# Performance work log

Hardware: AMD Instinct MI355X
Metric: run time of the kernel (lower is better)

Reference implementation:

```python
import jax, jax.numpy as jnp
import numpy as np

B, L, H = 2, 1024, 1024   # batch, seq_len, hidden_size
NH, D, K = 16, 64, 4      # num_heads, head_dim, conv kernel
HD = NH * D


def setup_inputs() -> dict:
    key = jax.random.key(0)
    ks = jax.random.split(key, 12)
    s = 0.02  # LeCun-ish init scale as in the torch module
    return {
        "hidden_states": jax.random.normal(ks[0], (B, L, H), jnp.float32),
        "Wq": jax.random.normal(ks[1], (HD, H), jnp.float32) * s,
        "bq": jnp.zeros((HD,), jnp.float32),
        "Wk": jax.random.normal(ks[2], (HD, H), jnp.float32) * s,
        "bk": jnp.zeros((HD,), jnp.float32),
        "Wv": jax.random.normal(ks[3], (HD, H), jnp.float32) * s,
        "bv": jnp.zeros((HD,), jnp.float32),
        "Wa": jax.random.normal(ks[4], (NH, H), jnp.float32) * s,
        "Wb": jax.random.normal(ks[5], (NH, H), jnp.float32) * s,
        "Wconv": jax.random.normal(ks[6], (HD, 1, K), jnp.float32) * s,
        "Wo": jax.random.normal(ks[7], (H, HD), jnp.float32) * s,
        "bo": jnp.zeros((H,), jnp.float32),
    }


def _gated_delta(q, k, v, alpha, beta):
    # q,k,v: [B,L,NH,D]; alpha,beta: [B,L,NH]
    # S_t = S_{t-1} @ (alpha_t * (I - beta_t k_t k_t^T)) + beta_t v_t k_t^T ; o_t = S_t q_t
    eye = jnp.eye(q.shape[-1], dtype=q.dtype)

    def step(S, xs):
        q_t, k_t, v_t, a_t, b_t = xs  # [B,NH,D], [B,NH]
        kk = jnp.einsum('bhd,bhe->bhde', k_t, k_t)
        decay = a_t[..., None, None] * (eye - b_t[..., None, None] * kk)
        S = jnp.einsum('bhde,bhef->bhdf', S, decay) \
            + b_t[..., None, None] * jnp.einsum('bhd,bhe->bhde', v_t, k_t)
        o_t = jnp.einsum('bhde,bhe->bhd', S, q_t)
        return S, o_t

    xs = (jnp.moveaxis(q, 1, 0), jnp.moveaxis(k, 1, 0), jnp.moveaxis(v, 1, 0),
          jnp.moveaxis(alpha, 1, 0), jnp.moveaxis(beta, 1, 0))
    S0 = jnp.zeros((q.shape[0], q.shape[2], q.shape[3], q.shape[3]), q.dtype)
    _, outs = jax.lax.scan(step, S0, xs)  # [L,B,NH,D]
    return jnp.transpose(outs, (1, 2, 0, 3))  # [B,NH,L,D] (matches torch stack+transposes)


def reference(hidden_states, Wq, bq, Wk, bk, Wv, bv, Wa, Wb, Wconv, Wo, bo):
    Bc, Lc, Hc = hidden_states.shape
    q = (hidden_states @ Wq.T + bq).reshape(Bc, Lc, NH, D)
    k = (hidden_states @ Wk.T + bk).reshape(Bc, Lc, NH, D)
    v = (hidden_states @ Wv.T + bv).reshape(Bc, Lc, NH, D)
    alpha = jax.nn.sigmoid(hidden_states @ Wa.T)   # [B,L,NH]
    beta = jax.nn.softplus(hidden_states @ Wb.T)   # [B,L,NH]

    out = _gated_delta(q, k, v, alpha, beta)       # [B,NH,L,D]
    out = out.reshape(Bc, Lc, NH * D)              # replicates torch's reshape of [B,NH,L,D]
    x = jnp.transpose(out, (0, 2, 1))              # [B,HD,L]
    conv = jax.lax.conv_general_dilated(
        x, Wconv, window_strides=(1,), padding=[(K - 1, 0)],
        feature_group_count=NH * D, dimension_numbers=('NCH', 'OIH', 'NCH'))
    x = x + conv                                   # residual depthwise causal conv
    x = jnp.transpose(x, (0, 2, 1))                # [B,L,HD]
    return x @ Wo.T + bo                           # [B,L,H]; dropout is identity at eval
```

## Files before the change

### kernel.cpp

```cpp
#include <hip/hip_runtime.h>
#include <math.h>

#define BB 2
#define LL 1024
#define HH 1024
#define NH 16
#define DD 64
#define HD (NH * DD)
#define MM (BB * LL)
#define RCT 32
#define KEXT 3072
#define NB_QKV 3200

typedef _Float16 f16x8 __attribute__((ext_vector_type(8)));
typedef _Float16 f16x4 __attribute__((ext_vector_type(4)));
typedef float f32x4 __attribute__((ext_vector_type(4)));

__device__ __forceinline__ void load_lds16(const void* g, void* l) {
    __builtin_amdgcn_global_load_lds(
        (const __attribute__((address_space(1))) void*)g,
        (__attribute__((address_space(3))) void*)l, 16, 0, 0);
}

__global__ __launch_bounds__(256) void convert_front(
    const float* __restrict__ hs,
    const float* __restrict__ Wq, const float* __restrict__ Wk,
    const float* __restrict__ Wv, const float* __restrict__ Wa,
    const float* __restrict__ Wb, const float* __restrict__ Wo,
    _Float16* __restrict__ Ae, _Float16* __restrict__ Be,
    _Float16* __restrict__ Be2)
{
    const int blk = blockIdx.x;
    const int t = threadIdx.x;

    if (blk >= 5248) {
        const int n = blk - 5248;
        float4 x = *(const float4*)(Wo + (size_t)n * 1024 + t * 4);
        f16x4 h;
        h[0] = (_Float16)(x.x * 64.f);
        h[1] = (_Float16)(x.y * 64.f);
        h[2] = (_Float16)(x.z * 64.f);
        h[3] = (_Float16)(x.w * 64.f);
        *(f16x4*)(Be2 + (size_t)n * 1024 + t * 4) = h;
        return;
    }

    const float* src = nullptr;
    _Float16* dst;
    float scale;
    bool a_side;
    if (blk < 2048) {
        src = hs + (size_t)blk * 1024;
        dst = Ae + (size_t)blk * KEXT;
        scale = 16.f; a_side = true;
    } else {
        const int n = blk - 2048;
        if (n < 1024)      src = Wq + (size_t)n * 1024;
        else if (n < 2048) src = Wk + (size_t)(n - 1024) * 1024;
        else if (n < 3072) src = Wv + (size_t)(n - 2048) * 1024;
        else if (n < 3088) src = Wa + (size_t)(n - 3072) * 1024;
        else if (n < 3104) src = Wb + (size_t)(n - 3088) * 1024;
        dst = Be + (size_t)n * KEXT;
        scale = 64.f; a_side = false;
    }
    float4 x = src ? *(const float4*)(src + t * 4) : make_float4(0.f,0.f,0.f,0.f);
    x.x *= scale; x.y *= scale; x.z *= scale; x.w *= scale;
    f16x4 h, l;
    h[0] = (_Float16)x.x; l[0] = (_Float16)(x.x - (float)h[0]);
    h[1] = (_Float16)x.y; l[1] = (_Float16)(x.y - (float)h[1]);
    h[2] = (_Float16)x.z; l[2] = (_Float16)(x.z - (float)h[2]);
    h[3] = (_Float16)x.w; l[3] = (_Float16)(x.w - (float)h[3]);
    _Float16* base = dst + t * 4;
    *(f16x4*)(base)        = h;
    *(f16x4*)(base + 1024) = a_side ? l : h;
    *(f16x4*)(base + 2048) = a_side ? h : l;
}

__global__ __launch_bounds__(256) void mfma_gemm_qkv(
    const _Float16* __restrict__ Ae, const _Float16* __restrict__ Be,
    float* __restrict__ qkv, float* __restrict__ ab,
    const float* __restrict__ bq, const float* __restrict__ bk,
    const float* __restrict__ bv)
{
    __shared__ __align__(16) _Float16 As[2][128 * 32];
    __shared__ __align__(16) _Float16 Bs[2][128 * 32];

    const int tid = threadIdx.x;
    const int wave = tid >> 6;
    const int lane = tid & 63;
    const int bm = blockIdx.y * 128;
    const int bn = blockIdx.x * 128;
    const int wr = (wave >> 1) * 64;
    const int wc = (wave & 1) * 64;

    const int srow = lane >> 2;
    const int scol = (lane & 3) * 8;
    const _Float16* gA0 = Ae + (size_t)(bm + wave * 32 + srow) * KEXT + scol;
    const _Float16* gA1 = gA0 + (size_t)16 * KEXT;
    const _Float16* gB0 = Be + (size_t)(bn + wave * 32 + srow) * KEXT + scol;
    const _Float16* gB1 = gB0 + (size_t)16 * KEXT;
    _Float16* lA0_0 = &As[0][(wave * 32) * 32];
    _Float16* lA1_0 = &As[0][(wave * 32 + 16) * 32];
    _Float16* lB0_0 = &Bs[0][(wave * 32) * 32];
    _Float16* lB1_0 = &Bs[0][(wave * 32 + 16) * 32];
    _Float16* lA0_1 = &As[1][(wave * 32) * 32];
    _Float16* lA1_1 = &As[1][(wave * 32 + 16) * 32];
    _Float16* lB0_1 = &Bs[1][(wave * 32) * 32];
    _Float16* lB1_1 = &Bs[1][(wave * 32 + 16) * 32];

    const int fm = lane & 15;
    const int fq = (lane >> 4) * 8;

    f32x4 acc[4][4] = {};

    for (int k0 = 0; k0 < KEXT; k0 += 64) {
        load_lds16(gA0 + k0,      lA0_0);
        load_lds16(gA1 + k0,      lA1_0);
        load_lds16(gB0 + k0,      lB0_0);
        load_lds16(gB1 + k0,      lB1_0);
        load_lds16(gA0 + k0 + 32, lA0_1);
        load_lds16(gA1 + k0 + 32, lA1_1);
        load_lds16(gB0 + k0 + 32, lB0_1);
        load_lds16(gB1 + k0 + 32, lB1_1);
        __syncthreads();

        #pragma unroll
        for (int s = 0; s < 2; ++s) {
            f16x8 a[4], b[4];
            #pragma unroll
            for (int mt = 0; mt < 4; ++mt)
                a[mt] = *(const f16x8*)&As[s][(wr + mt * 16 + fm) * 32 + fq];
            #pragma unroll
            for (int nt = 0; nt < 4; ++nt)
                b[nt] = *(const f16x8*)&Bs[s][(wc + nt * 16 + fm) * 32 + fq];
            #pragma unroll
            for (int mt = 0; mt < 4; ++mt)
                #pragma unroll
                for (int nt = 0; nt < 4; ++nt)
                    acc[mt][nt] = __builtin_amdgcn_mfma_f32_16x16x32_f16(
                        a[mt], b[nt], acc[mt][nt], 0, 0, 0);
        }
        __syncthreads();
    }

    const int rquad = (lane >> 4) * 4;
    #pragma unroll
    for (int mt = 0; mt < 4; ++mt) {
        #pragma unroll
        for (int nt = 0; nt < 4; ++nt) {
            const int col = bn + wc + nt * 16 + fm;
            #pragma unroll
            for (int i = 0; i < 4; ++i) {
                const int row = bm + wr + mt * 16 + rquad + i;
                float val = acc[mt][nt][i] * (1.0f / 1024.0f);
                if (col < 1024)
                    qkv[(size_t)row * 3072 + col] = val + bq[col];
                else if (col < 2048)
                    qkv[(size_t)row * 3072 + col] = val + bk[col - 1024];
                else if (col < 3072)
                    qkv[(size_t)row * 3072 + col] = val + bv[col - 2048];
                else {
                    const int c = col - 3072;
                    if (c < 16)
                        ab[(size_t)row * 32 + c] = 1.f / (1.f + expf(-val));
                    else if (c < 32)
                        ab[(size_t)row * 32 + c] =
                            fmaxf(val, 0.f) + log1pf(expf(-fabsf(val)));
                }
            }
        }
    }
}

__global__ __launch_bounds__(256) void mfma_gemm_out(
    const _Float16* __restrict__ Ae2, const _Float16* __restrict__ Be2,
    float* __restrict__ outp, const float* __restrict__ bo)
{
    __shared__ __align__(16) _Float16 As[2][128 * 32];
    __shared__ __align__(16) _Float16 Bs[2][64 * 32];

    const int tid = threadIdx.x;
    const int wave = tid >> 6;
    const int lane = tid & 63;
    const int bm = blockIdx.y * 128;
    const int bn = blockIdx.x * 64;
    const int wr = (wave >> 1) * 64;
    const int wc = (wave & 1) * 32;

    const int srow = lane >> 2;
    const int scol = (lane & 3) * 8;
    const _Float16* gA0 = Ae2 + (size_t)(bm + wave * 32 + srow) * 1024 + scol;
    const _Float16* gA1 = gA0 + (size_t)16 * 1024;
    const _Float16* gB0 = Be2 + (size_t)(bn + wave * 16 + srow) * 1024 + scol;
    _Float16* lA0_0 = &As[0][(wave * 32) * 32];
    _Float16* lA1_0 = &As[0][(wave * 32 + 16) * 32];
    _Float16* lB0_0 = &Bs[0][(wave * 16) * 32];
    _Float16* lA0_1 = &As[1][(wave * 32) * 32];
    _Float16* lA1_1 = &As[1][(wave * 32 + 16) * 32];
    _Float16* lB0_1 = &Bs[1][(wave * 16) * 32];

    const int fm = lane & 15;
    const int fq = (lane >> 4) * 8;

    f32x4 acc[4][2] = {};

    for (int k0 = 0; k0 < 1024; k0 += 64) {
        load_lds16(gA0 + k0,      lA0_0);
        load_lds16(gA1 + k0,      lA1_0);
        load_lds16(gB0 + k0,      lB0_0);
        load_lds16(gA0 + k0 + 32, lA0_1);
        load_lds16(gA1 + k0 + 32, lA1_1);
        load_lds16(gB0 + k0 + 32, lB0_1);
        __syncthreads();

        #pragma unroll
        for (int s = 0; s < 2; ++s) {
            f16x8 a[4], b[2];
            #pragma unroll
            for (int mt = 0; mt < 4; ++mt)
                a[mt] = *(const f16x8*)&As[s][(wr + mt * 16 + fm) * 32 + fq];
            #pragma unroll
            for (int nt = 0; nt < 2; ++nt)
                b[nt] = *(const f16x8*)&Bs[s][(wc + nt * 16 + fm) * 32 + fq];
            #pragma unroll
            for (int mt = 0; mt < 4; ++mt)
                #pragma unroll
                for (int nt = 0; nt < 2; ++nt)
                    acc[mt][nt] = __builtin_amdgcn_mfma_f32_16x16x32_f16(
                        a[mt], b[nt], acc[mt][nt], 0, 0, 0);
        }
        __syncthreads();
    }

    const int rquad = (lane >> 4) * 4;
    #pragma unroll
    for (int mt = 0; mt < 4; ++mt) {
        #pragma unroll
        for (int nt = 0; nt < 2; ++nt) {
            const int col = bn + wc + nt * 16 + fm;
            #pragma unroll
            for (int i = 0; i < 4; ++i) {
                const int row = bm + wr + mt * 16 + rquad + i;
                outp[(size_t)row * 1024 + col] = acc[mt][nt][i] * 64.f + bo[col];
            }
        }
    }
}

template <int CTRL>
__device__ __forceinline__ float dpp_addf(float x) {
    int y = __builtin_amdgcn_update_dpp(0, __builtin_bit_cast(int, x),
                                        CTRL, 0xF, 0xF, true);
    return x + __builtin_bit_cast(float, y);
}
__device__ __forceinline__ float red16(float x) {
    x = dpp_addf<0xB1>(x);
    x = dpp_addf<0x4E>(x);
    x = dpp_addf<0x124>(x);
    x = dpp_addf<0x128>(x);
    return x;
}

__global__ __launch_bounds__(64) void gdn_recurrence(
    const float* __restrict__ qkv, const float* __restrict__ ab,
    float* __restrict__ att)
{
    __shared__ __align__(16) float ks[2][RCT][64];
    __shared__ __align__(16) float qs[2][RCT][64];
    __shared__ __align__(16) float vs_[2][RCT][4];
    __shared__ __align__(16) float gab[2][RCT][2];

    const int blk = blockIdx.x;
    const int bh = blk & 31;
    const int s  = blk >> 5;
    const int b  = bh >> 4;
    const int h  = bh & 15;
    const int lane = threadIdx.x;
    const int rl = lane >> 4;
    const int el = lane & 15;
    const int e0 = el * 4;
    const int r0 = s * 4;

    const float* qb  = qkv + (size_t)b * LL * 3072 + h * 64;
    const float* kb  = qb + 1024;
    const float* vb  = qb + 2048 + r0;
    const float* abp = ab + (size_t)b * LL * 32 + h;
    float* op = att + ((size_t)(b * NH + h) * DD + r0 + rl) * LL;

    const int st = lane >> 4;
    const int sd = (lane & 15) * 4;

    float S0 = 0.f, S1 = 0.f, S2 = 0.f, S3 = 0.f;

    {
        const size_t ro = (size_t)st * 3072 + sd;
        #pragma unroll
        for (int m = 0; m < 8; ++m) {
            load_lds16(kb + ro + (size_t)m * 4 * 3072, &ks[0][m * 4][0]);
            load_lds16(qb + ro + (size_t)m * 4 * 3072, &qs[0][m * 4][0]);
        }
        float4 pv = make_float4(0.f,0.f,0.f,0.f);
        if (lane < RCT) pv = *(const float4*)(vb + (size_t)lane * 3072);
        float pab = (lane < 32) ? abp[(size_t)lane * 32]
                                : abp[(size_t)(lane - 32) * 32 + 16];
        if (lane < RCT) *(float4*)&vs_[0][lane][0] = pv;
        if (lane < 32) gab[0][lane][0] = pab;
        else           gab[0][lane - 32][1] = pab;
    }
    __syncthreads();

    const int NCHUNK = LL / RCT;
    for (int c = 0; c < NCHUNK; ++c) {
        const int cur = c & 1, nxt = cur ^ 1;
        const bool more = (c + 1 < NCHUNK);

        float4 pv = make_float4(0.f,0.f,0.f,0.f);
        float pab = 0.f;
        if (more) {
            const size_t t0 = (size_t)(c + 1) * RCT;
            const size_t ro = (t0 + st) * 3072 + sd;
            #pragma unroll
            for (int m = 0; m < 8; ++m) {
                load_lds16(kb + ro + (size_t)m * 4 * 3072, &ks[nxt][m * 4][0]);
                load_lds16(qb + ro + (size_t)m * 4 * 3072, &qs[nxt][m * 4][0]);
            }
            if (lane < RCT) pv = *(const float4*)(vb + (t0 + lane) * 3072);
            pab = (lane < 32) ? abp[(t0 + lane) * 32]
                              : abp[(t0 + lane - 32) * 32 + 16];
        }

        float4 kc = *(const float4*)&ks[cur][0][e0];
        float4 qc = *(const float4*)&qs[cur][0][e0];
        float vc = vs_[cur][0][rl];
        float2 abc = *(const float2*)&gab[cur][0][0];
        float ac = abc.x;
        float bc = abc.y;

        float o0 = 0.f, o1 = 0.f, o2 = 0.f;
        #pragma unroll 4
        for (int t = 0; t < RCT; ++t) {
            const int tn = (t + 1) & (RCT - 1);
            float4 kn = *(const float4*)&ks[cur][tn][e0];
            float4 qn = *(const float4*)&qs[cur][tn][e0];
            const float vn = vs_[cur][tn][rl];
            const float2 abn = *(const float2*)&gab[cur][tn][0];

            float p0 = fmaf(S1, kc.y, S0 * kc.x);
            float p1 = fmaf(S3, kc.w, S2 * kc.z);
            float sk = red16(p0 + p1);

            const float cf = bc * fmaf(-ac, sk, vc);

            S0 = fmaf(ac, S0, cf * kc.x);
            S1 = fmaf(ac, S1, cf * kc.y);
            S2 = fmaf(ac, S2, cf * kc.z);
            S3 = fmaf(ac, S3, cf * kc.w);

            float q0 = fmaf(S1, qc.y, S0 * qc.x);
            float q1 = fmaf(S3, qc.w, S2 * qc.z);
            float o = red16(q0 + q1);

            const int ph = t & 3;
            if (ph == 0) o0 = o;
            else if (ph == 1) o1 = o;
            else if (ph == 2) o2 = o;
            else if (el == 0)
                *(float4*)(op + c * RCT + t - 3) = make_float4(o0, o1, o2, o);

            kc = kn; qc = qn; vc = vn; ac = abn.x; bc = abn.y;
        }

        if (more) {
            if (lane < RCT) *(float4*)&vs_[nxt][lane][0] = pv;
            if (lane < 32) gab[nxt][lane][0] = pab;
            else           gab[nxt][lane - 32][1] = pab;
        }
        __syncthreads();
    }
}

__global__ __launch_bounds__(256) void conv_convert(
    const float* __restrict__ att, const float* __restrict__ Wconv,
    _Float16* __restrict__ Ae2)
{
    __shared__ float yt[112][68];
    const int lb = blockIdx.x;
    const int h  = blockIdx.y;
    const int b  = blockIdx.z;
    const int tid = threadIdx.x;

    {
        const int d = tid >> 2;
        const int part = tid & 3;
        const float* src  = att + ((size_t)(b * NH + h) * DD + d) * LL;
        const float* srcm = src - (size_t)DD * LL;
        #pragma unroll
        for (int m = 0; m < 7; ++m) {
            const int off = (part * 7 + m) * 4;
            const int lg = lb * 64 - 48 + off;
            float4 v;
            if (lg >= 0)      v = *(const float4*)(src + lg);
            else if (h > 0)   v = *(const float4*)(srcm + lg + 1024);
            else              v = make_float4(0.f, 0.f, 0.f, 0.f);
            yt[off + 0][d] = v.x; yt[off + 1][d] = v.y;
            yt[off + 2][d] = v.z; yt[off + 3][d] = v.w;
        }
    }
    __syncthreads();

    float4 w[4];
    #pragma unroll
    for (int k = 0; k < 4; ++k)
        w[k] = ((const float4*)Wconv)[tid * 4 + k];

    const int d0 = (tid & 15) * 4;
    const int lq = tid >> 4;
    const float sc = 1.f / 4096.f;

    #pragma unroll
    for (int rr = 0; rr < 4; ++rr) {
        const int ll = rr * 16 + lq;
        float y0[4], y1[4], y2[4], y3[4];
        *(float4*)y0 = *(const float4*)&yt[ll +  0][d0];
        *(float4*)y1 = *(const float4*)&yt[ll + 16][d0];
        *(float4*)y2 = *(const float4*)&yt[ll + 32][d0];
        *(float4*)y3 = *(const float4*)&yt[ll + 48][d0];
        f16x4 hi;
        #pragma unroll
        for (int k = 0; k < 4; ++k) {
            float acc = y3[k];
            acc = fmaf(w[k].x, y0[k], acc);
            acc = fmaf(w[k].y, y1[k], acc);
            acc = fmaf(w[k].z, y2[k], acc);
            acc = fmaf(w[k].w, y3[k], acc);
            hi[k] = (_Float16)(acc * sc);
        }
        const size_t row = (size_t)b * 1024 + h * 64 + lb * 4 + rr;
        *(f16x4*)(Ae2 + row * 1024 + tid * 4) = hi;
    }
}

extern "C" void kernel_launch(void* const* d_in, const int* in_sizes, int n_in,
                              void* d_out, int out_size, void* d_ws, size_t ws_size,
                              hipStream_t stream)
{
    const float* hs    = (const float*)d_in[0];
    const float* Wq    = (const float*)d_in[1];
    const float* bq    = (const float*)d_in[2];
    const float* Wk    = (const float*)d_in[3];
    const float* bk    = (const float*)d_in[4];
    const float* Wv    = (const float*)d_in[5];
    const float* bv    = (const float*)d_in[6];
    const float* Wa    = (const float*)d_in[7];
    const float* Wb    = (const float*)d_in[8];
    const float* Wconv = (const float*)d_in[9];
    const float* Wo    = (const float*)d_in[10];
    const float* bo    = (const float*)d_in[11];
    float* out = (float*)d_out;

    char* w = (char*)d_ws;
    float* qkv = (float*)w;        w += (size_t)MM * 3072 * 4;
    float* att = (float*)w;        w += (size_t)MM * 1024 * 4;
    float* ab  = (float*)w;        w += (size_t)MM * 32 * 4;
    _Float16* Ae  = (_Float16*)w;  w += (size_t)MM * KEXT * 2;
    _Float16* Be  = (_Float16*)w;  w += (size_t)NB_QKV * KEXT * 2;
    _Float16* Ae2 = (_Float16*)w;  w += (size_t)MM * 1024 * 2;
    _Float16* Be2 = (_Float16*)w;  w += (size_t)1024 * 1024 * 2;

    hipLaunchKernelGGL(convert_front, dim3(2048 + NB_QKV + 1024), dim3(256), 0, stream,
                       hs, Wq, Wk, Wv, Wa, Wb, Wo, Ae, Be, Be2);

    hipLaunchKernelGGL(mfma_gemm_qkv, dim3(NB_QKV / 128, MM / 128), dim3(256), 0, stream,
                       Ae, Be, qkv, ab, bq, bk, bv);

    hipLaunchKernelGGL(gdn_recurrence, dim3(512), dim3(64), 0, stream, qkv, ab, att);

    hipLaunchKernelGGL(conv_convert, dim3(16, 16, BB), dim3(256), 0, stream,
                       att, Wconv, Ae2);

    hipLaunchKernelGGL(mfma_gemm_out, dim3(1024 / 64, MM / 128), dim3(256), 0, stream,
                       Ae2, Be2, out, bo);
}
```

Baseline: 307.4 us.

## Use split-fp16 precision only for K/alpha/beta projections, plain fp16 for Q and V

Splits the fused QKV projection GEMM into two GEMMs. The K, alpha and beta projections keep the 3x-extended K dimension (hi/lo fp16 split) for near-fp32 accuracy. The Q and V projections use a single fp16 pass with K=1024. This removes about two thirds of the MFMA work and global traffic for Q and V, at the cost of lower precision in those outputs and an extra kernel launch.

Measured after the change: 310.6 us. No clear change (+1.0%).

```diff
diff --git a/kernel.cpp b/kernel.cpp
--- a/kernel.cpp
+++ b/kernel.cpp
@@ -10,7 +10,7 @@
 #define MM (BB * LL)
 #define RCT 32
 #define KEXT 3072
-#define NB_QKV 3200
+#define NBK 1152
 
 typedef _Float16 f16x8 __attribute__((ext_vector_type(8)));
 typedef _Float16 f16x4 __attribute__((ext_vector_type(4)));
@@ -27,13 +27,62 @@
     const float* __restrict__ Wq, const float* __restrict__ Wk,
     const float* __restrict__ Wv, const float* __restrict__ Wa,
     const float* __restrict__ Wb, const float* __restrict__ Wo,
-    _Float16* __restrict__ Ae, _Float16* __restrict__ Be,
+    _Float16* __restrict__ Ae3, _Float16* __restrict__ Ah,
+    _Float16* __restrict__ Bk, _Float16* __restrict__ Bqv,
     _Float16* __restrict__ Be2)
 {
     const int blk = blockIdx.x;
     const int t = threadIdx.x;
 
-    if (blk >= 5248) {
+    if (blk < 2048) {
+        float4 x = *(const float4*)(hs + (size_t)blk * 1024 + t * 4);
+        x.x *= 16.f; x.y *= 16.f; x.z *= 16.f; x.w *= 16.f;
+        f16x4 h, l;
+        h[0] = (_Float16)x.x; l[0] = (_Float16)(x.x - (float)h[0]);
+        h[1] = (_Float16)x.y; l[1] = (_Float16)(x.y - (float)h[1]);
+        h[2] = (_Float16)x.z; l[2] = (_Float16)(x.z - (float)h[2]);
+        h[3] = (_Float16)x.w; l[3] = (_Float16)(x.w - (float)h[3]);
+        _Float16* base = Ae3 + (size_t)blk * KEXT + t * 4;
+        *(f16x4*)(base)        = h;
+        *(f16x4*)(base + 1024) = l;
+        *(f16x4*)(base + 2048) = h;
+        *(f16x4*)(Ah + (size_t)blk * 1024 + t * 4) = h;
+        return;
+    }
+    if (blk < 3200) {
+        const int n = blk - 2048;
+        const float* src = nullptr;
+        if (n < 1024)      src = Wk + (size_t)n * 1024;
+        else if (n < 1040) src = Wa + (size_t)(n - 1024) * 1024;
+        else if (n < 1056) src = Wb + (size_t)(n - 1040) * 1024;
+        float4 x = src ? *(const float4*)(src + t * 4)
+                       : make_float4(0.f, 0.f, 0.f, 0.f);
+        x.x *= 64.f; x.y *= 64.f; x.z *= 64.f; x.w *= 64.f;
+        f16x4 h, l;
+        h[0] = (_Float16)x.x; l[0] = (_Float16)(x.x - (float)h[0]);
+        h[1] = (_Float16)x.y; l[1] = (_Float16)(x.y - (float)h[1]);
+        h[2] = (_Float16)x.z; l[2] = (_Float16)(x.z - (float)h[2]);
+        h[3] = (_Float16)x.w; l[3] = (_Float16)(x.w - (float)h[3]);
+        _Float16* base = Bk + (size_t)n * KEXT + t * 4;
+        *(f16x4*)(base)        = h;
+        *(f16x4*)(base + 1024) = h;
+        *(f16x4*)(base + 2048) = l;
+        return;
+    }
+    if (blk < 5248) {
+        const int n = blk - 3200;
+        const float* src = (n < 1024) ? Wq + (size_t)n * 1024
+                                      : Wv + (size_t)(n - 1024) * 1024;
+        float4 x = *(const float4*)(src + t * 4);
+        f16x4 h;
+        h[0] = (_Float16)(x.x * 64.f);
+        h[1] = (_Float16)(x.y * 64.f);
+        h[2] = (_Float16)(x.z * 64.f);
+        h[3] = (_Float16)(x.w * 64.f);
+        *(f16x4*)(Bqv + (size_t)n * 1024 + t * 4) = h;
+        return;
+    }
+    {
         const int n = blk - 5248;
         float4 x = *(const float4*)(Wo + (size_t)n * 1024 + t * 4);
         f16x4 h;
@@ -42,45 +91,97 @@
         h[2] = (_Float16)(x.z * 64.f);
         h[3] = (_Float16)(x.w * 64.f);
         *(f16x4*)(Be2 + (size_t)n * 1024 + t * 4) = h;
-        return;
-    }
-
-    const float* src = nullptr;
-    _Float16* dst;
-    float scale;
-    bool a_side;
-    if (blk < 2048) {
-        src = hs + (size_t)blk * 1024;
-        dst = Ae + (size_t)blk * KEXT;
-        scale = 16.f; a_side = true;
-    } else {
-        const int n = blk - 2048;
-        if (n < 1024)      src = Wq + (size_t)n * 1024;
-        else if (n < 2048) src = Wk + (size_t)(n - 1024) * 1024;
-        else if (n < 3072) src = Wv + (size_t)(n - 2048) * 1024;
-        else if (n < 3088) src = Wa + (size_t)(n - 3072) * 1024;
-        else if (n < 3104) src = Wb + (size_t)(n - 3088) * 1024;
-        dst = Be + (size_t)n * KEXT;
-        scale = 64.f; a_side = false;
-    }
-    float4 x = src ? *(const float4*)(src + t * 4) : make_float4(0.f,0.f,0.f,0.f);
-    x.x *= scale; x.y *= scale; x.z *= scale; x.w *= scale;
-    f16x4 h, l;
-    h[0] = (_Float16)x.x; l[0] = (_Float16)(x.x - (float)h[0]);
-    h[1] = (_Float16)x.y; l[1] = (_Float16)(x.y - (float)h[1]);
-    h[2] = (_Float16)x.z; l[2] = (_Float16)(x.z - (float)h[2]);
-    h[3] = (_Float16)x.w; l[3] = (_Float16)(x.w - (float)h[3]);
-    _Float16* base = dst + t * 4;
-    *(f16x4*)(base)        = h;
-    *(f16x4*)(base + 1024) = a_side ? l : h;
-    *(f16x4*)(base + 2048) = a_side ? h : l;
-}
-
-__global__ __launch_bounds__(256) void mfma_gemm_qkv(
-    const _Float16* __restrict__ Ae, const _Float16* __restrict__ Be,
+    }
+}
+
+__global__ __launch_bounds__(256) void mfma_gemm_k(
+    const _Float16* __restrict__ Ae3, const _Float16* __restrict__ Bk,
     float* __restrict__ qkv, float* __restrict__ ab,
-    const float* __restrict__ bq, const float* __restrict__ bk,
-    const float* __restrict__ bv)
+    const float* __restrict__ bk)
+{
+    __shared__ __align__(16) _Float16 As[2][128 * 32];
+    __shared__ __align__(16) _Float16 Bs[2][64 * 32];
+
+    const int tid = threadIdx.x;
+    const int wave = tid >> 6;
+    const int lane = tid & 63;
+    const int bm = blockIdx.y * 128;
+    const int bn = blockIdx.x * 64;
+    const int wr = (wave >> 1) * 64;
+    const int wc = (wave & 1) * 32;
+
+    const int srow = lane >> 2;
+    const int scol = (lane & 3) * 8;
+    const _Float16* gA0 = Ae3 + (size_t)(bm + wave * 32 + srow) * KEXT + scol;
+    const _Float16* gA1 = gA0 + (size_t)16 * KEXT;
+    const _Float16* gB0 = Bk + (size_t)(bn + wave * 16 + srow) * KEXT + scol;
+    _Float16* lA0_0 = &As[0][(wave * 32) * 32];
+    _Float16* lA1_0 = &As[0][(wave * 32 + 16) * 32];
+    _Float16* lB0_0 = &Bs[0][(wave * 16) * 32];
+    _Float16* lA0_1 = &As[1][(wave * 32) * 32];
+    _Float16* lA1_1 = &As[1][(wave * 32 + 16) * 32];
+    _Float16* lB0_1 = &Bs[1][(wave * 16) * 32];
+
+    const int fm = lane & 15;
+    const int fq = (lane >> 4) * 8;
+
+    f32x4 acc[4][2] = {};
+
+    for (int k0 = 0; k0 < KEXT; k0 += 64) {
+        load_lds16(gA0 + k0,      lA0_0);
+        load_lds16(gA1 + k0,      lA1_0);
+        load_lds16(gB0 + k0,      lB0_0);
+        load_lds16(gA0 + k0 + 32, lA0_1);
+        load_lds16(gA1 + k0 + 32, lA1_1);
+        load_lds16(gB0 + k0 + 32, lB0_1);
+        __syncthreads();
+
+        #pragma unroll
+        for (int s = 0; s < 2; ++s) {
+            f16x8 a[4], b[2];
+            #pragma unroll
+            for (int mt = 0; mt < 4; ++mt)
+                a[mt] = *(const f16x8*)&As[s][(wr + mt * 16 + fm) * 32 + fq];
+            #pragma unroll
+            for (int nt = 0; nt < 2; ++nt)
+                b[nt] = *(const f16x8*)&Bs[s][(wc + nt * 16 + fm) * 32 + fq];
+            #pragma unroll
+            for (int mt = 0; mt < 4; ++mt)
+                #pragma unroll
+                for (int nt = 0; nt < 2; ++nt)
+                    acc[mt][nt] = __builtin_amdgcn_mfma_f32_16x16x32_f16(
+                        a[mt], b[nt], acc[mt][nt], 0, 0, 0);
+        }
+        __syncthreads();
+    }
+
+    const int rquad = (lane >> 4) * 4;
+    #pragma unroll
+    for (int mt = 0; mt < 4; ++mt) {
+        #pragma unroll
+        for (int nt = 0; nt < 2; ++nt) {
+            const int col = bn + wc + nt * 16 + fm;
+            #pragma unroll
+            for (int i = 0; i < 4; ++i) {
+                const int row = bm + wr + mt * 16 + rquad + i;
+                float val = acc[mt][nt][i] * (1.0f / 1024.0f);
+                if (col < 1024)
+                    qkv[(size_t)row * 3072 + 1024 + col] = val + bk[col];
+                else if (col < 1040)
+                    ab[(size_t)row * 32 + (col - 1024)] =
+                        1.f / (1.f + expf(-val));
+                else if (col < 1056)
+                    ab[(size_t)row * 32 + 16 + (col - 1040)] =
+                        fmaxf(val, 0.f) + log1pf(expf(-fabsf(val)));
+            }
+        }
+    }
+}
+
+__global__ __launch_bounds__(256) void mfma_gemm_qv(
+    const _Float16* __restrict__ Ah, const _Float16* __restrict__ Bqv,
+    float* __restrict__ qkv,
+    const float* __restrict__ bq, const float* __restrict__ bv)
 {
     __shared__ __align__(16) _Float16 As[2][128 * 32];
     __shared__ __align__(16) _Float16 Bs[2][128 * 32];
@@ -95,10 +196,10 @@
 
     const int srow = lane >> 2;
     const int scol = (lane & 3) * 8;
-    const _Float16* gA0 = Ae + (size_t)(bm + wave * 32 + srow) * KEXT + scol;
-    const _Float16* gA1 = gA0 + (size_t)16 * KEXT;
-    const _Float16* gB0 = Be + (size_t)(bn + wave * 32 + srow) * KEXT + scol;
-    const _Float16* gB1 = gB0 + (size_t)16 * KEXT;
+    const _Float16* gA0 = Ah + (size_t)(bm + wave * 32 + srow) * 1024 + scol;
+    const _Float16* gA1 = gA0 + (size_t)16 * 1024;
+    const _Float16* gB0 = Bqv + (size_t)(bn + wave * 32 + srow) * 1024 + scol;
+    const _Float16* gB1 = gB0 + (size_t)16 * 1024;
     _Float16* lA0_0 = &As[0][(wave * 32) * 32];
     _Float16* lA1_0 = &As[0][(wave * 32 + 16) * 32];
     _Float16* lB0_0 = &Bs[0][(wave * 32) * 32];
@@ -113,7 +214,7 @@
 
     f32x4 acc[4][4] = {};
 
-    for (int k0 = 0; k0 < KEXT; k0 += 64) {
+    for (int k0 = 0; k0 < 1024; k0 += 64) {
         load_lds16(gA0 + k0,      lA0_0);
         load_lds16(gA1 + k0,      lA1_0);
         load_lds16(gB0 + k0,      lB0_0);
@@ -155,18 +256,8 @@
                 float val = acc[mt][nt][i] * (1.0f / 1024.0f);
                 if (col < 1024)
                     qkv[(size_t)row * 3072 + col] = val + bq[col];
-                else if (col < 2048)
-                    qkv[(size_t)row * 3072 + col] = val + bk[col - 1024];
-                else if (col < 3072)
-                    qkv[(size_t)row * 3072 + col] = val + bv[col - 2048];
-                else {
-                    const int c = col - 3072;
-                    if (c < 16)
-                        ab[(size_t)row * 32 + c] = 1.f / (1.f + expf(-val));
-                    else if (c < 32)
-                        ab[(size_t)row * 32 + c] =
-                            fmaxf(val, 0.f) + log1pf(expf(-fabsf(val)));
-                }
+                else
+                    qkv[(size_t)row * 3072 + 1024 + col] = val + bv[col - 1024];
             }
         }
     }
@@ -462,16 +553,21 @@
     float* qkv = (float*)w;        w += (size_t)MM * 3072 * 4;
     float* att = (float*)w;        w += (size_t)MM * 1024 * 4;
     float* ab  = (float*)w;        w += (size_t)MM * 32 * 4;
-    _Float16* Ae  = (_Float16*)w;  w += (size_t)MM * KEXT * 2;
-    _Float16* Be  = (_Float16*)w;  w += (size_t)NB_QKV * KEXT * 2;
+    _Float16* Ae3 = (_Float16*)w;  w += (size_t)MM * KEXT * 2;
+    _Float16* Ah  = (_Float16*)w;  w += (size_t)MM * 1024 * 2;
+    _Float16* Bk  = (_Float16*)w;  w += (size_t)NBK * KEXT * 2;
+    _Float16* Bqv = (_Float16*)w;  w += (size_t)2048 * 1024 * 2;
     _Float16* Ae2 = (_Float16*)w;  w += (size_t)MM * 1024 * 2;
     _Float16* Be2 = (_Float16*)w;  w += (size_t)1024 * 1024 * 2;
 
-    hipLaunchKernelGGL(convert_front, dim3(2048 + NB_QKV + 1024), dim3(256), 0, stream,
-                       hs, Wq, Wk, Wv, Wa, Wb, Wo, Ae, Be, Be2);
-
-    hipLaunchKernelGGL(mfma_gemm_qkv, dim3(NB_QKV / 128, MM / 128), dim3(256), 0, stream,
-                       Ae, Be, qkv, ab, bq, bk, bv);
+    hipLaunchKernelGGL(convert_front, dim3(6272), dim3(256), 0, stream,
+                       hs, Wq, Wk, Wv, Wa, Wb, Wo, Ae3, Ah, Bk, Bqv, Be2);
+
+    hipLaunchKernelGGL(mfma_gemm_k, dim3(NBK / 64, MM / 128), dim3(256), 0, stream,
+                       Ae3, Bk, qkv, ab, bk);
+
+    hipLaunchKernelGGL(mfma_gemm_qv, dim3(2048 / 128, MM / 128), dim3(256), 0, stream,
+                       Ah, Bqv, qkv, bq, bv);
 
     hipLaunchKernelGGL(gdn_recurrence, dim3(512), dim3(64), 0, stream, qkv, ab, att);
 
```
